# Optimization experiments

Measured on AMD Instinct MI355X. Metric: run time of the kernel, lower is better.

Reference implementation:

```python
import jax, jax.numpy as jnp
import numpy as np

B, T, H, L, V = 1024, 200, 128, 2, 100001


def setup_inputs() -> dict:
    key = jax.random.key(0)
    ks = jax.random.split(key, 10)
    s = 1.0 / np.sqrt(H).astype(np.float32)  # PyTorch GRU init range
    return {
        "interaction_list": jax.random.randint(ks[0], (B, T), 0, V),
        "interaction_mask": jax.random.randint(ks[1], (B, T), 0, 2).astype(jnp.float32),
        "neg_list": jax.random.randint(ks[2], (B, T), 0, V),
        "emb": jax.random.normal(ks[3], (V, H), dtype=jnp.float32) * 0.02,
        "Wih": jax.random.uniform(ks[4], (L, 3 * H, H), minval=-s, maxval=s, dtype=jnp.float32),
        "Whh": jax.random.uniform(ks[5], (L, 3 * H, H), minval=-s, maxval=s, dtype=jnp.float32),
        "bih": jax.random.uniform(ks[6], (L, 3 * H), minval=-s, maxval=s, dtype=jnp.float32),
        "bhh": jax.random.uniform(ks[7], (L, 3 * H), minval=-s, maxval=s, dtype=jnp.float32),
        "h2o_w": jax.random.uniform(ks[8], (H, H), minval=-s, maxval=s, dtype=jnp.float32),
        "h2o_b": jax.random.uniform(ks[9], (H,), minval=-s, maxval=s, dtype=jnp.float32),
    }


def _gru_cell(x, h, Wih_l, Whh_l, bih_l, bhh_l):
    # PyTorch GRU gate math; gi/gh: [B, 3H]
    gi = x @ Wih_l.T + bih_l
    gh = h @ Whh_l.T + bhh_l
    ir, iz, inn = jnp.split(gi, 3, axis=-1)
    hr, hz, hn = jnp.split(gh, 3, axis=-1)
    r = jax.nn.sigmoid(ir + hr)
    z = jax.nn.sigmoid(iz + hz)
    n = jnp.tanh(inn + r * hn)
    return (1.0 - z) * n + z * h


def _run_gru(input_embs, mask, Wih, Whh, bih, bhh, h2o_w, h2o_b):
    x_seq = input_embs.transpose(1, 0, 2)  # [T, B, H]
    m_seq = mask.transpose(1, 0)           # [T, B]

    def step(hidden, xm):
        x, m = xm
        hs = []
        for l in range(L):  # fixed small layer count
            h = _gru_cell(x, hidden[l], Wih[l], Whh[l], bih[l], bhh[l])
            hs.append(h)
            x = h
        out = jnp.tanh(x @ h2o_w.T + h2o_b)  # h2o + tanh head (per step)
        keep = (m != 0.0).astype(x.dtype)    # mask hidden AFTER output
        hidden = jnp.stack(hs) * keep[None, :, None]
        return hidden, out

    h0 = jnp.zeros((L, B, H), dtype=input_embs.dtype)
    _, outs = jax.lax.scan(step, h0, (x_seq, m_seq))  # outs: [T, B, H]
    return outs.transpose(1, 0, 2)  # [B, T, H]


def reference(interaction_list, interaction_mask, neg_list, emb, Wih, Whh, bih, bhh, h2o_w, h2o_b):
    input_embs_all = emb[interaction_list]            # [B, T, H]
    target_pos_embs = input_embs_all[:, 1:, :]        # [B, T-1, H]
    target_neg_embs = emb[neg_list][:, :-1, :]        # [B, T-1, H]
    final_output = _run_gru(input_embs_all, interaction_mask, Wih, Whh, bih, bhh, h2o_w, h2o_b)
    return (
        final_output[:, :-1, :],
        target_pos_embs,
        target_neg_embs,
        jnp.concatenate((input_embs_all, final_output), axis=2),
    )
```

## Files before the change

### kernel.cpp

```cpp
#include <hip/hip_runtime.h>

#define Bsz 1024
#define Tt 200
#define Hh 128
#define Gg 384
#define OUT0_SZ (1024L*199*128)

#define WSEG 49152
#define WTOT (4*WSEG + 16384)

typedef _Float16 half8 __attribute__((ext_vector_type(8)));
typedef float floatx4 __attribute__((ext_vector_type(4)));

#define BAR() asm volatile("s_waitcnt lgkmcnt(0)\n\ts_barrier" ::: "memory")

__device__ __forceinline__ float fsigm(float x) {
    return __builtin_amdgcn_rcpf(1.f + __expf(-x));
}
__device__ __forceinline__ float ftanh(float x) {
    float e = __expf(2.f * x);
    return 1.f - 2.f * __builtin_amdgcn_rcpf(e + 1.f);
}

__global__ void pack_weights(const float* __restrict__ Wih, const float* __restrict__ Whh,
                             const float* __restrict__ h2o_w, ushort* __restrict__ wbuf) {
    int idx = blockIdx.x * blockDim.x + threadIdx.x;
    if (idx >= WTOT) return;
    const float* src; int off;
    if      (idx <   WSEG) { src = Wih;            off = idx;          }
    else if (idx < 2*WSEG) { src = Whh;            off = idx -   WSEG; }
    else if (idx < 3*WSEG) { src = Wih + Gg*Hh;    off = idx - 2*WSEG; }
    else if (idx < 4*WSEG) { src = Whh + Gg*Hh;    off = idx - 3*WSEG; }
    else                   { src = h2o_w;          off = idx - 4*WSEG; }
    int j    = off & 7;
    int lane = (off >> 3) & 63;
    int kt   = (off >> 9) & 3;
    int tile = off >> 11;
    int n = tile*16 + (lane & 15);
    int k = kt*32 + (lane >> 4)*8 + j;
    union { _Float16 h; ushort u; } cv;
    cv.h = (_Float16)src[n*Hh + k];
    wbuf[idx] = cv.u;
}

__global__ __launch_bounds__(512) void gru_fused(
    const int* __restrict__ il, const float* __restrict__ mask,
    const int* __restrict__ negl, const float* __restrict__ emb,
    const float* __restrict__ bih, const float* __restrict__ bhh,
    const float* __restrict__ h2o_b, const ushort* __restrict__ wbuf,
    float* __restrict__ out)
{
    __shared__ _Float16 xa_lds[2][16*136];
    __shared__ _Float16 x1_lds[16*136];
    __shared__ _Float16 h0_lds[16*136];
    __shared__ _Float16 h1_lds[16*136];
    __shared__ float    g_lds[16*516];
    __shared__ float    brz_s[2*256];
    __shared__ float    bin_s[2*128];
    __shared__ float    bhn_s[2*128];
    __shared__ float    bo_s[128];
    __shared__ int      il_s[16*Tt];
    __shared__ float    keep_f[16*Tt];

    const int tid = threadIdx.x;
    float* out0 = out;
    float* out1 = out + OUT0_SZ;
    float* out2 = out + 2*OUT0_SZ;
    float* out3 = out + 3*OUT0_SZ;

    if (blockIdx.x >= 64) {
        const float4* emb4 = (const float4*)emb;
        float4* o1 = (float4*)out1;
        float4* o2 = (float4*)out2;
        float4* o3 = (float4*)out3;
        const int nA = 1024*200*32;
        const int nB = 1024*199*32;
        const int total = nA + 2*nB;
        const int stride = 192*512;
        for (int i = (blockIdx.x - 64)*512 + tid; i < total; i += stride) {
            if (i < nA) {
                int c = i & 31; int bt = i >> 5;
                int e = il[bt];
                o3[bt*64 + c] = emb4[(long)e*32 + c];
            } else if (i < nA + nB) {
                int ii = i - nA; int c = ii & 31; int bt = ii >> 5;
                int b = bt / 199, t = bt - b*199;
                int e = il[b*Tt + t + 1];
                o1[bt*32 + c] = emb4[(long)e*32 + c];
            } else {
                int ii = i - nA - nB; int c = ii & 31; int bt = ii >> 5;
                int b = bt / 199, t = bt - b*199;
                int e = negl[b*Tt + t];
                o2[bt*32 + c] = emb4[(long)e*32 + c];
            }
        }
        return;
    }

    const int wave = tid >> 6;
    const int lane = tid & 63;
    const int b0   = blockIdx.x * 16;
    const int col  = lane & 15;
    const int q    = lane >> 4;
    const int arow = (lane & 15)*136;
    const int koffq = (lane >> 4)*8;

    { int l = tid >> 8, n = tid & 255; brz_s[tid] = bih[l*Gg + n] + bhh[l*Gg + n]; }
    if (tid < 256) { int l = tid >> 7, jj = tid & 127; bin_s[tid] = bih[l*Gg + 256 + jj]; bhn_s[tid] = bhh[l*Gg + 256 + jj]; }
    if (tid < 128) bo_s[tid] = h2o_b[tid];
    for (int i = tid; i < 16*136; i += 512) { h0_lds[i] = (_Float16)0.f; h1_lds[i] = (_Float16)0.f; }
    for (int i = tid; i < 16*Tt; i += 512) {
        int r = i / Tt, c = i - r*Tt;
        il_s[i]   = il[(b0 + r)*Tt + c];
        keep_f[i] = (mask[(b0 + r)*Tt + c] != 0.f) ? 1.f : 0.f;
    }

    const half8* wb = (const half8*)wbuf;
    half8 wih0[3][4], whh0[3][4];
#pragma unroll
    for (int s = 0; s < 3; s++) {
        const int tl = (s == 0) ? wave : (s == 1) ? (8 + wave) : (16 + wave);
#pragma unroll
        for (int k = 0; k < 4; k++) {
            wih0[s][k] = wb[0*6144 + (tl*4 + k)*64 + lane];
            whh0[s][k] = wb[1*6144 + (tl*4 + k)*64 + lane];
        }
    }

    {
        int r = tid >> 5, c4 = tid & 31;
        int e = il[(b0 + r)*Tt];
        float4 v = ((const float4*)emb)[(long)e*32 + c4];
        _Float16* dst = &xa_lds[0][r*136 + c4*4];
        dst[0] = (_Float16)v.x; dst[1] = (_Float16)v.y;
        dst[2] = (_Float16)v.z; dst[3] = (_Float16)v.w;
    }
    __syncthreads();

    const int r5 = tid >> 5, c4g = tid & 31;

    for (int t = 0; t < Tt; t++) {
        _Float16* cur = xa_lds[t & 1];
        _Float16* nxt = xa_lds[(t + 1) & 1];

        float4 pv;
        if (t < Tt - 1) {
            int e = il_s[r5*Tt + t + 1];
            pv = ((const float4*)emb)[(long)e*32 + c4g];
        }

        half8 p_w1r[4], p_w1z[4], p_w1n[4], p_whr[4], p_whz[4], p_whn[4];
        {
            floatx4 acc_r = {0.f,0.f,0.f,0.f}, acc_z = {0.f,0.f,0.f,0.f};
            floatx4 acc_in = {0.f,0.f,0.f,0.f}, acc_hn = {0.f,0.f,0.f,0.f};
#pragma unroll
            for (int k = 0; k < 4; k++) {
                half8 xf = *(const half8*)&cur[arow + k*32 + koffq];
                half8 hf = *(const half8*)&h0_lds[arow + k*32 + koffq];
                acc_r  = __builtin_amdgcn_mfma_f32_16x16x32_f16(xf, wih0[0][k], acc_r, 0, 0, 0);
                acc_r  = __builtin_amdgcn_mfma_f32_16x16x32_f16(hf, whh0[0][k], acc_r, 0, 0, 0);
                acc_z  = __builtin_amdgcn_mfma_f32_16x16x32_f16(xf, wih0[1][k], acc_z, 0, 0, 0);
                acc_z  = __builtin_amdgcn_mfma_f32_16x16x32_f16(hf, whh0[1][k], acc_z, 0, 0, 0);
                acc_in = __builtin_amdgcn_mfma_f32_16x16x32_f16(xf, wih0[2][k], acc_in, 0, 0, 0);
                acc_hn = __builtin_amdgcn_mfma_f32_16x16x32_f16(hf, whh0[2][k], acc_hn, 0, 0, 0);
            }
#pragma unroll
            for (int r2 = 0; r2 < 4; r2++) {
                int row = q*4 + r2;
                g_lds[row*516 +       wave*16 + col] = acc_r[r2];
                g_lds[row*516 + 128 + wave*16 + col] = acc_z[r2];
                g_lds[row*516 + 256 + wave*16 + col] = acc_in[r2];
                g_lds[row*516 + 384 + wave*16 + col] = acc_hn[r2];
            }
#pragma unroll
            for (int k = 0; k < 4; k++) {
                p_w1r[k] = wb[2*6144 + (( 0 + wave)*4 + k)*64 + lane];
                p_w1z[k] = wb[2*6144 + (( 8 + wave)*4 + k)*64 + lane];
                p_w1n[k] = wb[2*6144 + ((16 + wave)*4 + k)*64 + lane];
                p_whr[k] = wb[3*6144 + (( 0 + wave)*4 + k)*64 + lane];
                p_whz[k] = wb[3*6144 + (( 8 + wave)*4 + k)*64 + lane];
                p_whn[k] = wb[3*6144 + ((16 + wave)*4 + k)*64 + lane];
            }
        }
        BAR();

        {
            int jj = tid & 127, bq = tid >> 7;
#pragma unroll
            for (int itr = 0; itr < 4; itr++) {
                int b = itr*4 + bq;
                float gr  = g_lds[b*516 +       jj] + brz_s[jj];
                float gz  = g_lds[b*516 + 128 + jj] + brz_s[128 + jj];
                float gin = g_lds[b*516 + 256 + jj] + bin_s[jj];
                float ghn = g_lds[b*516 + 384 + jj] + bhn_s[jj];
                float rr = fsigm(gr);
                float zz = fsigm(gz);
                float nn = ftanh(gin + rr*ghn);
                float hp = (float)h0_lds[b*136 + jj];
                float hv = (1.f - zz)*nn + zz*hp;
                x1_lds[b*136 + jj] = (_Float16)hv;
                h0_lds[b*136 + jj] = (_Float16)(hv * keep_f[b*Tt + t]);
            }
        }
        BAR();

        half8 p_o[4];
        {
            floatx4 acc_r = {0.f,0.f,0.f,0.f}, acc_z = {0.f,0.f,0.f,0.f};
            floatx4 acc_in = {0.f,0.f,0.f,0.f}, acc_hn = {0.f,0.f,0.f,0.f};
#pragma unroll
            for (int k = 0; k < 4; k++) {
                half8 xf = *(const half8*)&x1_lds[arow + k*32 + koffq];
                half8 hf = *(const half8*)&h1_lds[arow + k*32 + koffq];
                acc_r  = __builtin_amdgcn_mfma_f32_16x16x32_f16(xf, p_w1r[k], acc_r, 0, 0, 0);
                acc_r  = __builtin_amdgcn_mfma_f32_16x16x32_f16(hf, p_whr[k], acc_r, 0, 0, 0);
                acc_z  = __builtin_amdgcn_mfma_f32_16x16x32_f16(xf, p_w1z[k], acc_z, 0, 0, 0);
                acc_z  = __builtin_amdgcn_mfma_f32_16x16x32_f16(hf, p_whz[k], acc_z, 0, 0, 0);
                acc_in = __builtin_amdgcn_mfma_f32_16x16x32_f16(xf, p_w1n[k], acc_in, 0, 0, 0);
                acc_hn = __builtin_amdgcn_mfma_f32_16x16x32_f16(hf, p_whn[k], acc_hn, 0, 0, 0);
            }
#pragma unroll
            for (int r2 = 0; r2 < 4; r2++) {
                int row = q*4 + r2;
                g_lds[row*516 +       wave*16 + col] = acc_r[r2];
                g_lds[row*516 + 128 + wave*16 + col] = acc_z[r2];
                g_lds[row*516 + 256 + wave*16 + col] = acc_in[r2];
                g_lds[row*516 + 384 + wave*16 + col] = acc_hn[r2];
            }
#pragma unroll
            for (int k = 0; k < 4; k++) p_o[k] = wb[4*6144 + (wave*4 + k)*64 + lane];
        }
        BAR();

        {
            int jj = tid & 127, bq = tid >> 7;
#pragma unroll
            for (int itr = 0; itr < 4; itr++) {
                int b = itr*4 + bq;
                float gr  = g_lds[b*516 +       jj] + brz_s[256 + jj];
                float gz  = g_lds[b*516 + 128 + jj] + brz_s[256 + 128 + jj];
                float gin = g_lds[b*516 + 256 + jj] + bin_s[128 + jj];
                float ghn = g_lds[b*516 + 384 + jj] + bhn_s[128 + jj];
                float rr = fsigm(gr);
                float zz = fsigm(gz);
                float nn = ftanh(gin + rr*ghn);
                float hp = (float)h1_lds[b*136 + jj];
                float hv = (1.f - zz)*nn + zz*hp;
                cur[b*136 + jj]    = (_Float16)hv;
                h1_lds[b*136 + jj] = (_Float16)(hv * keep_f[b*Tt + t]);
            }
            if (t < Tt - 1) {
                _Float16* dst = &nxt[r5*136 + c4g*4];
                dst[0] = (_Float16)pv.x; dst[1] = (_Float16)pv.y;
                dst[2] = (_Float16)pv.z; dst[3] = (_Float16)pv.w;
            }
        }
        BAR();

        {
            floatx4 acc_o = {0.f,0.f,0.f,0.f};
#pragma unroll
            for (int k = 0; k < 4; k++) {
                half8 xf = *(const half8*)&cur[arow + k*32 + koffq];
                acc_o = __builtin_amdgcn_mfma_f32_16x16x32_f16(xf, p_o[k], acc_o, 0, 0, 0);
            }
            int nout = wave*16 + col;
            float bs = bo_s[nout];
#pragma unroll
            for (int r2 = 0; r2 < 4; r2++) {
                int brow = q*4 + r2;
                float v = ftanh(acc_o[r2] + bs);
                out3[((long)(b0 + brow)*Tt + t)*256 + 128 + nout] = v;
                if (t < Tt - 1) out0[((long)(b0 + brow)*199 + t)*128 + nout] = v;
            }
        }
    }
}

extern "C" void kernel_launch(void* const* d_in, const int* in_sizes, int n_in,
                              void* d_out, int out_size, void* d_ws, size_t ws_size,
                              hipStream_t stream) {
    const int*   il    = (const int*)  d_in[0];
    const float* msk   = (const float*)d_in[1];
    const int*   negl  = (const int*)  d_in[2];
    const float* emb   = (const float*)d_in[3];
    const float* Wih   = (const float*)d_in[4];
    const float* Whh   = (const float*)d_in[5];
    const float* bih   = (const float*)d_in[6];
    const float* bhh   = (const float*)d_in[7];
    const float* h2o_w = (const float*)d_in[8];
    const float* h2o_b = (const float*)d_in[9];
    float* out = (float*)d_out;
    ushort* wbuf = (ushort*)d_ws;

    pack_weights<<<(WTOT + 255)/256, 256, 0, stream>>>(Wih, Whh, h2o_w, wbuf);
    gru_fused<<<256, 512, 0, stream>>>(il, msk, negl, emb, bih, bhh, h2o_b, wbuf, out);
}
```

Measured before the change: 1.359 ms.

## Compute GRU gates in MFMA registers and defer output head to cut barriers

Gate nonlinearities are now applied directly on the MFMA accumulator fragments in registers, so the g_lds staging round trip is gone. Hidden state is kept in registers and written to double-buffered LDS in a fragment-native layout. The h2o output projection for step t-1 is overlapped with layer-0 work at step t, and embedding prefetch runs one step further ahead. Together these reduce the per-timestep barriers from four to two, at the cost of higher register pressure and more complex index math (with launch_bounds now requesting 2 blocks).

```diff
diff --git a/kernel.cpp b/kernel.cpp
--- a/kernel.cpp
+++ b/kernel.cpp
@@ -13,6 +13,8 @@
 typedef float floatx4 __attribute__((ext_vector_type(4)));
 
 #define BAR() asm volatile("s_waitcnt lgkmcnt(0)\n\ts_barrier" ::: "memory")
+
+#define MFMA16(A, B, C) __builtin_amdgcn_mfma_f32_16x16x32_f16((A), (B), (C), 0, 0, 0)
 
 __device__ __forceinline__ float fsigm(float x) {
     return __builtin_amdgcn_rcpf(1.f + __expf(-x));
@@ -43,24 +45,19 @@
     wbuf[idx] = cv.u;
 }
 
-__global__ __launch_bounds__(512) void gru_fused(
+__global__ __launch_bounds__(512, 2) void gru_fused(
     const int* __restrict__ il, const float* __restrict__ mask,
     const int* __restrict__ negl, const float* __restrict__ emb,
     const float* __restrict__ bih, const float* __restrict__ bhh,
     const float* __restrict__ h2o_b, const ushort* __restrict__ wbuf,
     float* __restrict__ out)
 {
-    __shared__ _Float16 xa_lds[2][16*136];
-    __shared__ _Float16 x1_lds[16*136];
-    __shared__ _Float16 h0_lds[16*136];
-    __shared__ _Float16 h1_lds[16*136];
-    __shared__ float    g_lds[16*516];
-    __shared__ float    brz_s[2*256];
-    __shared__ float    bin_s[2*128];
-    __shared__ float    bhn_s[2*128];
-    __shared__ float    bo_s[128];
-    __shared__ int      il_s[16*Tt];
-    __shared__ float    keep_f[16*Tt];
+    __shared__ half8 xa_f[2][256];
+    __shared__ half8 x1_f[256];
+    __shared__ half8 h0_f[2][256];
+    __shared__ half8 h1_f[2][256];
+    __shared__ int   il_s[16*Tt];
+    __shared__ float keep_s[16*Tt];
 
     const int tid = threadIdx.x;
     float* out0 = out;
@@ -100,23 +97,38 @@
     const int wave = tid >> 6;
     const int lane = tid & 63;
     const int b0   = blockIdx.x * 16;
-    const int col  = lane & 15;
+    const int cl   = lane & 15;
     const int q    = lane >> 4;
-    const int arow = (lane & 15)*136;
-    const int koffq = (lane >> 4)*8;
-
-    { int l = tid >> 8, n = tid & 255; brz_s[tid] = bih[l*Gg + n] + bhh[l*Gg + n]; }
-    if (tid < 256) { int l = tid >> 7, jj = tid & 127; bin_s[tid] = bih[l*Gg + 256 + jj]; bhn_s[tid] = bhh[l*Gg + 256 + jj]; }
-    if (tid < 128) bo_s[tid] = h2o_b[tid];
-    for (int i = tid; i < 16*136; i += 512) { h0_lds[i] = (_Float16)0.f; h1_lds[i] = (_Float16)0.f; }
+    const int col  = wave*16 + cl;
+
+    const int hidx0 = ((wave >> 1)*64 + ((wave & 1)*2 + (cl >> 3))*16 + q*4)*8 + (cl & 7);
+
+    const int r5 = tid >> 5, c4 = tid & 31;
+    const int ebase = ((c4 >> 3)*64 + ((c4 & 7) >> 1)*16 + r5)*8 + (c4 & 1)*4;
+
     for (int i = tid; i < 16*Tt; i += 512) {
         int r = i / Tt, c = i - r*Tt;
         il_s[i]   = il[(b0 + r)*Tt + c];
-        keep_f[i] = (mask[(b0 + r)*Tt + c] != 0.f) ? 1.f : 0.f;
-    }
+        keep_s[i] = (mask[(b0 + r)*Tt + c] != 0.f) ? 1.f : 0.f;
+    }
+    {
+        _Float16* z0 = (_Float16*)h0_f;
+        _Float16* z1 = (_Float16*)h1_f;
+        for (int i = tid; i < 4096; i += 512) { z0[i] = (_Float16)0.f; z1[i] = (_Float16)0.f; }
+    }
+
+    const float br0 = bih[col]       + bhh[col];
+    const float bz0 = bih[128 + col] + bhh[128 + col];
+    const float bi0 = bih[256 + col];
+    const float bh0 = bhh[256 + col];
+    const float br1 = bih[384 + col]       + bhh[384 + col];
+    const float bz1 = bih[384 + 128 + col] + bhh[384 + 128 + col];
+    const float bi1 = bih[384 + 256 + col];
+    const float bh1 = bhh[384 + 256 + col];
+    const float bo  = h2o_b[col];
 
     const half8* wb = (const half8*)wbuf;
-    half8 wih0[3][4], whh0[3][4];
+    half8 wih0[3][4], whh0[3][4], p_o[4];
 #pragma unroll
     for (int s = 0; s < 3; s++) {
         const int tl = (s == 0) ? wave : (s == 1) ? (8 + wave) : (16 + wave);
@@ -126,153 +138,142 @@
             whh0[s][k] = wb[1*6144 + (tl*4 + k)*64 + lane];
         }
     }
-
+#pragma unroll
+    for (int k = 0; k < 4; k++) p_o[k] = wb[4*6144 + (wave*4 + k)*64 + lane];
+
+    const float4* emb4v = (const float4*)emb;
     {
-        int r = tid >> 5, c4 = tid & 31;
-        int e = il[(b0 + r)*Tt];
-        float4 v = ((const float4*)emb)[(long)e*32 + c4];
-        _Float16* dst = &xa_lds[0][r*136 + c4*4];
-        dst[0] = (_Float16)v.x; dst[1] = (_Float16)v.y;
-        dst[2] = (_Float16)v.z; dst[3] = (_Float16)v.w;
-    }
+        int e = il[(b0 + r5)*Tt];
+        float4 v = emb4v[(long)e*32 + c4];
+        _Float16* d = (_Float16*)xa_f[0];
+        d[ebase]   = (_Float16)v.x; d[ebase+1] = (_Float16)v.y;
+        d[ebase+2] = (_Float16)v.z; d[ebase+3] = (_Float16)v.w;
+    }
+    float4 pv;
+    { int e = il[(b0 + r5)*Tt + 1]; pv = emb4v[(long)e*32 + c4]; }
+
+    float hprev0[4] = {0.f,0.f,0.f,0.f};
+    float hprev1[4] = {0.f,0.f,0.f,0.f};
     __syncthreads();
 
-    const int r5 = tid >> 5, c4g = tid & 31;
-
     for (int t = 0; t < Tt; t++) {
-        _Float16* cur = xa_lds[t & 1];
-        _Float16* nxt = xa_lds[(t + 1) & 1];
-
-        float4 pv;
-        if (t < Tt - 1) {
-            int e = il_s[r5*Tt + t + 1];
-            pv = ((const float4*)emb)[(long)e*32 + c4g];
-        }
-
+        float k4[4];
+#pragma unroll
+        for (int r2 = 0; r2 < 4; r2++) k4[r2] = keep_s[(q*4 + r2)*Tt + t];
+
+        const half8* xcur = xa_f[t & 1];
+        const half8* hcur = h0_f[t & 1];
+        floatx4 acc_r = {0,0,0,0}, acc_z = {0,0,0,0}, acc_in = {0,0,0,0}, acc_hn = {0,0,0,0};
+#pragma unroll
+        for (int k = 0; k < 4; k++) {
+            half8 xf = xcur[k*64 + lane];
+            half8 hf = hcur[k*64 + lane];
+            acc_r  = MFMA16(xf, wih0[0][k], acc_r);
+            acc_r  = MFMA16(hf, whh0[0][k], acc_r);
+            acc_z  = MFMA16(xf, wih0[1][k], acc_z);
+            acc_z  = MFMA16(hf, whh0[1][k], acc_z);
+            acc_in = MFMA16(xf, wih0[2][k], acc_in);
+            acc_hn = MFMA16(hf, whh0[2][k], acc_hn);
+        }
+        floatx4 acc_o = {0,0,0,0};
+        if (t > 0) {
+            const half8* hx = xa_f[(t + 1) & 1];
+#pragma unroll
+            for (int k = 0; k < 4; k++) acc_o = MFMA16(hx[k*64 + lane], p_o[k], acc_o);
+        }
         half8 p_w1r[4], p_w1z[4], p_w1n[4], p_whr[4], p_whz[4], p_whn[4];
+#pragma unroll
+        for (int k = 0; k < 4; k++) {
+            p_w1r[k] = wb[2*6144 + (( 0 + wave)*4 + k)*64 + lane];
+            p_w1z[k] = wb[2*6144 + (( 8 + wave)*4 + k)*64 + lane];
+            p_w1n[k] = wb[2*6144 + ((16 + wave)*4 + k)*64 + lane];
+            p_whr[k] = wb[3*6144 + (( 0 + wave)*4 + k)*64 + lane];
+            p_whz[k] = wb[3*6144 + (( 8 + wave)*4 + k)*64 + lane];
+            p_whn[k] = wb[3*6144 + ((16 + wave)*4 + k)*64 + lane];
+        }
         {
-            floatx4 acc_r = {0.f,0.f,0.f,0.f}, acc_z = {0.f,0.f,0.f,0.f};
-            floatx4 acc_in = {0.f,0.f,0.f,0.f}, acc_hn = {0.f,0.f,0.f,0.f};
-#pragma unroll
-            for (int k = 0; k < 4; k++) {
-                half8 xf = *(const half8*)&cur[arow + k*32 + koffq];
-                half8 hf = *(const half8*)&h0_lds[arow + k*32 + koffq];
-                acc_r  = __builtin_amdgcn_mfma_f32_16x16x32_f16(xf, wih0[0][k], acc_r, 0, 0, 0);
-                acc_r  = __builtin_amdgcn_mfma_f32_16x16x32_f16(hf, whh0[0][k], acc_r, 0, 0, 0);
-                acc_z  = __builtin_amdgcn_mfma_f32_16x16x32_f16(xf, wih0[1][k], acc_z, 0, 0, 0);
-                acc_z  = __builtin_amdgcn_mfma_f32_16x16x32_f16(hf, whh0[1][k], acc_z, 0, 0, 0);
-                acc_in = __builtin_amdgcn_mfma_f32_16x16x32_f16(xf, wih0[2][k], acc_in, 0, 0, 0);
-                acc_hn = __builtin_amdgcn_mfma_f32_16x16x32_f16(hf, whh0[2][k], acc_hn, 0, 0, 0);
-            }
+            _Float16* x1h = (_Float16*)x1_f;
+            _Float16* h0n = (_Float16*)h0_f[(t + 1) & 1];
 #pragma unroll
             for (int r2 = 0; r2 < 4; r2++) {
-                int row = q*4 + r2;
-                g_lds[row*516 +       wave*16 + col] = acc_r[r2];
-                g_lds[row*516 + 128 + wave*16 + col] = acc_z[r2];
-                g_lds[row*516 + 256 + wave*16 + col] = acc_in[r2];
-                g_lds[row*516 + 384 + wave*16 + col] = acc_hn[r2];
-            }
-#pragma unroll
-            for (int k = 0; k < 4; k++) {
-                p_w1r[k] = wb[2*6144 + (( 0 + wave)*4 + k)*64 + lane];
-                p_w1z[k] = wb[2*6144 + (( 8 + wave)*4 + k)*64 + lane];
-                p_w1n[k] = wb[2*6144 + ((16 + wave)*4 + k)*64 + lane];
-                p_whr[k] = wb[3*6144 + (( 0 + wave)*4 + k)*64 + lane];
-                p_whz[k] = wb[3*6144 + (( 8 + wave)*4 + k)*64 + lane];
-                p_whn[k] = wb[3*6144 + ((16 + wave)*4 + k)*64 + lane];
-            }
-        }
-        BAR();
-
-        {
-            int jj = tid & 127, bq = tid >> 7;
-#pragma unroll
-            for (int itr = 0; itr < 4; itr++) {
-                int b = itr*4 + bq;
-                float gr  = g_lds[b*516 +       jj] + brz_s[jj];
-                float gz  = g_lds[b*516 + 128 + jj] + brz_s[128 + jj];
-                float gin = g_lds[b*516 + 256 + jj] + bin_s[jj];
-                float ghn = g_lds[b*516 + 384 + jj] + bhn_s[jj];
+                float gr = acc_r[r2]  + br0;
+                float gz = acc_z[r2]  + bz0;
+                float gn = acc_in[r2] + bi0;
+                float gh = acc_hn[r2] + bh0;
                 float rr = fsigm(gr);
                 float zz = fsigm(gz);
-                float nn = ftanh(gin + rr*ghn);
-                float hp = (float)h0_lds[b*136 + jj];
-                float hv = (1.f - zz)*nn + zz*hp;
-                x1_lds[b*136 + jj] = (_Float16)hv;
-                h0_lds[b*136 + jj] = (_Float16)(hv * keep_f[b*Tt + t]);
+                float nn = ftanh(gn + rr*gh);
+                float hv = (1.f - zz)*nn + zz*hprev0[r2];
+                x1h[hidx0 + r2*8] = (_Float16)hv;
+                hprev0[r2] = hv * k4[r2];
+                h0n[hidx0 + r2*8] = (_Float16)hprev0[r2];
+            }
+        }
+        if (t > 0) {
+            int tt = t - 1;
+#pragma unroll
+            for (int r2 = 0; r2 < 4; r2++) {
+                int brow = q*4 + r2;
+                float v = ftanh(acc_o[r2] + bo);
+                out3[((long)(b0 + brow)*Tt + tt)*256 + 128 + col] = v;
+                out0[((long)(b0 + brow)*199 + tt)*128 + col] = v;
             }
         }
         BAR();
 
-        half8 p_o[4];
+        const half8* h1cur = h1_f[t & 1];
+        floatx4 b_r = {0,0,0,0}, b_z = {0,0,0,0}, b_in = {0,0,0,0}, b_hn = {0,0,0,0};
+#pragma unroll
+        for (int k = 0; k < 4; k++) {
+            half8 xf = x1_f[k*64 + lane];
+            half8 hf = h1cur[k*64 + lane];
+            b_r  = MFMA16(xf, p_w1r[k], b_r);
+            b_r  = MFMA16(hf, p_whr[k], b_r);
+            b_z  = MFMA16(xf, p_w1z[k], b_z);
+            b_z  = MFMA16(hf, p_whz[k], b_z);
+            b_in = MFMA16(xf, p_w1n[k], b_in);
+            b_hn = MFMA16(hf, p_whn[k], b_hn);
+        }
         {
-            floatx4 acc_r = {0.f,0.f,0.f,0.f}, acc_z = {0.f,0.f,0.f,0.f};
-            floatx4 acc_in = {0.f,0.f,0.f,0.f}, acc_hn = {0.f,0.f,0.f,0.f};
-#pragma unroll
-            for (int k = 0; k < 4; k++) {
-                half8 xf = *(const half8*)&x1_lds[arow + k*32 + koffq];
-                half8 hf = *(const half8*)&h1_lds[arow + k*32 + koffq];
-                acc_r  = __builtin_amdgcn_mfma_f32_16x16x32_f16(xf, p_w1r[k], acc_r, 0, 0, 0);
-                acc_r  = __builtin_amdgcn_mfma_f32_16x16x32_f16(hf, p_whr[k], acc_r, 0, 0, 0);
-                acc_z  = __builtin_amdgcn_mfma_f32_16x16x32_f16(xf, p_w1z[k], acc_z, 0, 0, 0);
-                acc_z  = __builtin_amdgcn_mfma_f32_16x16x32_f16(hf, p_whz[k], acc_z, 0, 0, 0);
-                acc_in = __builtin_amdgcn_mfma_f32_16x16x32_f16(xf, p_w1n[k], acc_in, 0, 0, 0);
-                acc_hn = __builtin_amdgcn_mfma_f32_16x16x32_f16(hf, p_whn[k], acc_hn, 0, 0, 0);
-            }
+            _Float16* xah = (_Float16*)xa_f[t & 1];
+            _Float16* h1n = (_Float16*)h1_f[(t + 1) & 1];
 #pragma unroll
             for (int r2 = 0; r2 < 4; r2++) {
-                int row = q*4 + r2;
-                g_lds[row*516 +       wave*16 + col] = acc_r[r2];
-                g_lds[row*516 + 128 + wave*16 + col] = acc_z[r2];
-                g_lds[row*516 + 256 + wave*16 + col] = acc_in[r2];
-                g_lds[row*516 + 384 + wave*16 + col] = acc_hn[r2];
-            }
-#pragma unroll
-            for (int k = 0; k < 4; k++) p_o[k] = wb[4*6144 + (wave*4 + k)*64 + lane];
-        }
-        BAR();
-
-        {
-            int jj = tid & 127, bq = tid >> 7;
-#pragma unroll
-            for (int itr = 0; itr < 4; itr++) {
-                int b = itr*4 + bq;
-                float gr  = g_lds[b*516 +       jj] + brz_s[256 + jj];
-                float gz  = g_lds[b*516 + 128 + jj] + brz_s[256 + 128 + jj];
-                float gin = g_lds[b*516 + 256 + jj] + bin_s[128 + jj];
-                float ghn = g_lds[b*516 + 384 + jj] + bhn_s[128 + jj];
+                float gr = b_r[r2]  + br1;
+                float gz = b_z[r2]  + bz1;
+                float gn = b_in[r2] + bi1;
+                float gh = b_hn[r2] + bh1;
                 float rr = fsigm(gr);
                 float zz = fsigm(gz);
-                float nn = ftanh(gin + rr*ghn);
-                float hp = (float)h1_lds[b*136 + jj];
-                float hv = (1.f - zz)*nn + zz*hp;
-                cur[b*136 + jj]    = (_Float16)hv;
-                h1_lds[b*136 + jj] = (_Float16)(hv * keep_f[b*Tt + t]);
-            }
-            if (t < Tt - 1) {
-                _Float16* dst = &nxt[r5*136 + c4g*4];
-                dst[0] = (_Float16)pv.x; dst[1] = (_Float16)pv.y;
-                dst[2] = (_Float16)pv.z; dst[3] = (_Float16)pv.w;
-            }
+                float nn = ftanh(gn + rr*gh);
+                float hv = (1.f - zz)*nn + zz*hprev1[r2];
+                xah[hidx0 + r2*8] = (_Float16)hv;
+                hprev1[r2] = hv * k4[r2];
+                h1n[hidx0 + r2*8] = (_Float16)hprev1[r2];
+            }
+        }
+        if (t + 1 < Tt) {
+            _Float16* d = (_Float16*)xa_f[(t + 1) & 1];
+            d[ebase]   = (_Float16)pv.x; d[ebase+1] = (_Float16)pv.y;
+            d[ebase+2] = (_Float16)pv.z; d[ebase+3] = (_Float16)pv.w;
+        }
+        if (t + 2 < Tt) {
+            int e = il_s[r5*Tt + t + 2];
+            pv = emb4v[(long)e*32 + c4];
         }
         BAR();
-
-        {
-            floatx4 acc_o = {0.f,0.f,0.f,0.f};
-#pragma unroll
-            for (int k = 0; k < 4; k++) {
-                half8 xf = *(const half8*)&cur[arow + k*32 + koffq];
-                acc_o = __builtin_amdgcn_mfma_f32_16x16x32_f16(xf, p_o[k], acc_o, 0, 0, 0);
-            }
-            int nout = wave*16 + col;
-            float bs = bo_s[nout];
-#pragma unroll
-            for (int r2 = 0; r2 < 4; r2++) {
-                int brow = q*4 + r2;
-                float v = ftanh(acc_o[r2] + bs);
-                out3[((long)(b0 + brow)*Tt + t)*256 + 128 + nout] = v;
-                if (t < Tt - 1) out0[((long)(b0 + brow)*199 + t)*128 + nout] = v;
-            }
+    }
+
+    {
+        const half8* hx = xa_f[(Tt - 1) & 1];
+        floatx4 acc_o = {0,0,0,0};
+#pragma unroll
+        for (int k = 0; k < 4; k++) acc_o = MFMA16(hx[k*64 + lane], p_o[k], acc_o);
+#pragma unroll
+        for (int r2 = 0; r2 < 4; r2++) {
+            int brow = q*4 + r2;
+            float v = ftanh(acc_o[r2] + bo);
+            out3[((long)(b0 + brow)*Tt + (Tt - 1))*256 + 128 + col] = v;
         }
     }
 }
```

Measured after the change: 1.147 ms. 15.6% less time.
